# Performance work log

Hardware: AMD Instinct MI355X
Metric: run time of the kernel (lower is better)

Reference implementation:

```python
import jax, jax.numpy as jnp
import numpy as np


def _batched_histc(x, bins):
    # x: [N, ...] -> per-sample histogram over [0, 1], matching torch.histc semantics:
    # bin = floor(v * bins), v == 1.0 goes to last bin, values outside [0,1] ignored.
    N = x.shape[0]
    flat = x.reshape(N, -1)
    idx = jnp.clip((flat * bins).astype(jnp.int32), 0, bins - 1)  # [N, P]
    valid = ((flat >= 0.0) & (flat <= 1.0)).astype(x.dtype)
    gidx = (jnp.arange(N, dtype=jnp.int32)[:, None] * bins + idx).reshape(-1)
    counts = jax.ops.segment_sum(valid.reshape(-1), gidx, num_segments=N * bins)
    return counts.reshape(N, bins)


def _mlp(h, W1, b1, W2, b2, W3, b3, W4, b4):
    h = jax.nn.relu(h @ W1 + b1)
    h = jax.nn.relu(h @ W2 + b2)
    h = jax.nn.relu(h @ W3 + b3)
    return h @ W4 + b4  # [N, 1]


def setup_inputs() -> dict:
    key = jax.random.key(0)
    ks = jax.random.split(key, 5)
    bins = 128
    N, C, H, W = 128, 1, 1024, 1024
    x = jax.random.uniform(ks[0], (N, C, H, W), dtype=jnp.float32)
    def lin(k, fan_in, fan_out):
        s = 1.0 / np.sqrt(fan_in)
        return jax.random.uniform(k, (fan_in, fan_out), jnp.float32, -s, s)
    return {
        "x": x,
        "W1": lin(ks[1], bins, 32), "b1": jnp.zeros((32,), jnp.float32),
        "W2": lin(ks[2], 32, 64),   "b2": jnp.zeros((64,), jnp.float32),
        "W3": lin(ks[3], 64, 128),  "b3": jnp.zeros((128,), jnp.float32),
        "W4": lin(ks[4], 128, 1),   "b4": jnp.zeros((1,), jnp.float32),
        "bins": bins,
    }


def reference(x, W1, b1, W2, b2, W3, b3, W4, b4, bins):
    hst = _batched_histc(x, bins)                       # [N, bins]
    w = _mlp(hst, W1, b1, W2, b2, W3, b3, W4, b4)       # [N, 1]
    w = w[:, :, None, None]                             # [N, 1, 1, 1]
    return x * w
```

## Files before the change

### kernel.cpp

```cpp
#include <hip/hip_runtime.h>

#define N_IMG 128
#define BINS 128
#define HW_ELEMS (1 << 20)
#define PARTS 8
#define NBLOCKS (N_IMG * PARTS)
#define PART_ELEMS (HW_ELEMS / PARTS)
#define PART_V4 (PART_ELEMS / 4)
#define NCOPY 8
#define HPAD 132
#define WSTRIDE 16

typedef float f32x4 __attribute__((ext_vector_type(4)));

__device__ __forceinline__ void ag_store(int* p, int v) {
    __hip_atomic_store(p, v, __ATOMIC_RELAXED, __HIP_MEMORY_SCOPE_AGENT);
}
__device__ __forceinline__ int ag_load(const int* p) {
    return __hip_atomic_load(p, __ATOMIC_RELAXED, __HIP_MEMORY_SCOPE_AGENT);
}
__device__ __forceinline__ int rmw_inc(int* p) {
    return __hip_atomic_fetch_add(p, 1, __ATOMIC_RELAXED, __HIP_MEMORY_SCOPE_AGENT);
}
__device__ __forceinline__ void st_w64(unsigned long long* p, unsigned long long v) {
    __hip_atomic_store(p, v, __ATOMIC_RELAXED, __HIP_MEMORY_SCOPE_AGENT);
}
__device__ __forceinline__ unsigned long long ld_w64(const unsigned long long* p) {
    return __hip_atomic_load(p, __ATOMIC_RELAXED, __HIP_MEMORY_SCOPE_AGENT);
}

__global__ __launch_bounds__(256, 4) void fused_kernel(
    const float* __restrict__ x,
    const float* __restrict__ W1, const float* __restrict__ b1,
    const float* __restrict__ W2, const float* __restrict__ b2,
    const float* __restrict__ W3, const float* __restrict__ b3,
    const float* __restrict__ W4, const float* __restrict__ b4,
    float* __restrict__ out,
    int* __restrict__ parthist,
    int* __restrict__ done,
    unsigned long long* __restrict__ wflag)
{
    __shared__ int   lh[NCOPY * HPAD];
    __shared__ float h0[BINS], a1[32], a2[64], a3[BINS];
    __shared__ int   retsh;
    __shared__ float wbc;

    const int t    = threadIdx.x;
    const int cpy  = t >> 5;
    const int img  = blockIdx.x >> 3;
    const int part = blockIdx.x & (PARTS - 1);

    for (int i = t; i < NCOPY * HPAD; i += 256) lh[i] = 0;
    __syncthreads();

    const f32x4* src = (const f32x4*)(x + (size_t)img * HW_ELEMS
                                        + (size_t)part * PART_ELEMS);

    #pragma unroll 4
    for (int i = t; i < PART_V4; i += 256) {
        f32x4 v = src[i];
        #pragma unroll
        for (int k = 0; k < 4; ++k) {
            float f = v[k];
            if (f >= 0.0f && f <= 1.0f) {
                int b = (int)(f * 128.0f);
                b = b > 127 ? 127 : b;
                atomicAdd(&lh[cpy * HPAD + b], 1);
            }
        }
    }
    __syncthreads();

    if (t < BINS) {
        int s = 0;
        #pragma unroll
        for (int c = 0; c < NCOPY; ++c) s += lh[c * HPAD + t];
        ag_store(&parthist[((size_t)img * PARTS + part) * BINS + t], s);
    }
    __syncthreads();
    if (t == 0) retsh = rmw_inc(&done[img]);
    __syncthreads();

    if (retsh == PARTS - 1) {
        if (t < BINS) {
            int s = 0;
            #pragma unroll
            for (int p = 0; p < PARTS; ++p)
                s += ag_load(&parthist[((size_t)img * PARTS + p) * BINS + t]);
            h0[t] = (float)s;
        }
        __syncthreads();
        if (t < 32) {
            float acc = b1[t];
            #pragma unroll 8
            for (int i = 0; i < 128; ++i) acc += h0[i] * W1[i * 32 + t];
            a1[t] = fmaxf(acc, 0.0f);
        }
        __syncthreads();
        if (t < 64) {
            float acc = b2[t];
            #pragma unroll 8
            for (int i = 0; i < 32; ++i) acc += a1[i] * W2[i * 64 + t];
            a2[t] = fmaxf(acc, 0.0f);
        }
        __syncthreads();
        if (t < 128) {
            float acc = b3[t];
            #pragma unroll 8
            for (int i = 0; i < 64; ++i) acc += a2[i] * W3[i * 128 + t];
            a3[t] = fmaxf(acc, 0.0f);
        }
        __syncthreads();
        if (t < 64) {
            float p = a3[t] * W4[t] + a3[t + 64] * W4[t + 64];
            #pragma unroll
            for (int off = 32; off > 0; off >>= 1)
                p += __shfl_down(p, off, 64);
            if (t == 0) {
                unsigned long long fv =
                    ((unsigned long long)__float_as_uint(p + b4[0]) << 32) | 1ull;
                st_w64(&wflag[(size_t)img * WSTRIDE], fv);
            }
        }
    }

    if (t == 0) {
        unsigned long long fv;
        while (((fv = ld_w64(&wflag[(size_t)img * WSTRIDE])) & 1ull) == 0ull)
            __builtin_amdgcn_s_sleep(16);
        wbc = __uint_as_float((unsigned)(fv >> 32));
    }
    __syncthreads();
    const float w = wbc;

    f32x4* dst = (f32x4*)(out + (size_t)img * HW_ELEMS
                              + (size_t)part * PART_ELEMS);
    #pragma unroll 4
    for (int i = t; i < PART_V4; i += 256) {
        f32x4 v = src[i];
        v *= w;
        __builtin_nontemporal_store(v, &dst[i]);
    }
}

extern "C" void kernel_launch(void* const* d_in, const int* in_sizes, int n_in,
                              void* d_out, int out_size, void* d_ws, size_t ws_size,
                              hipStream_t stream) {
    const float* x  = (const float*)d_in[0];
    const float* W1 = (const float*)d_in[1];
    const float* b1 = (const float*)d_in[2];
    const float* W2 = (const float*)d_in[3];
    const float* b2 = (const float*)d_in[4];
    const float* W3 = (const float*)d_in[5];
    const float* b3 = (const float*)d_in[6];
    const float* W4 = (const float*)d_in[7];
    const float* b4 = (const float*)d_in[8];

    int* done = (int*)d_ws;
    unsigned long long* wflag = (unsigned long long*)(done + N_IMG);
    int* parthist = (int*)(wflag + (size_t)N_IMG * WSTRIDE);

    hipMemsetAsync(d_ws, 0,
                   N_IMG * sizeof(int) + (size_t)N_IMG * WSTRIDE * sizeof(unsigned long long),
                   stream);

    fused_kernel<<<NBLOCKS, 256, 0, stream>>>(x, W1, b1, W2, b2, W3, b3, W4, b4,
                                              (float*)d_out, parthist, done, wflag);
}
```

Baseline: 322.3 us.

## Schedule scaling tiles by weight completion order and use per-quad histogram copies

The scaling pass is no longer tied to the block's own image. Each finished image's weight is pushed into a ring in completion order, and all blocks pull 128 KB tiles from eight atomic counters and scale tiles of whichever images are ready. This is meant to stop blocks spinning while waiting for a specific image's MLP. The shared histogram is also split into 64 copies, one per 4 threads, to cut atomic contention. The cost is more shared memory per block, which may lower occupancy, plus extra global atomics and barriers per tile.

```diff
diff --git a/kernel.cpp b/kernel.cpp
--- a/kernel.cpp
+++ b/kernel.cpp
@@ -7,9 +7,14 @@
 #define NBLOCKS (N_IMG * PARTS)
 #define PART_ELEMS (HW_ELEMS / PARTS)
 #define PART_V4 (PART_ELEMS / 4)
-#define NCOPY 8
+#define NCOPY 64
 #define HPAD 132
-#define WSTRIDE 16
+#define TILES_PER_IMG 32
+#define TILE_ELEMS (HW_ELEMS / TILES_PER_IMG)
+#define TILE_V4 (TILE_ELEMS / 4)
+#define TOTAL_TILES (N_IMG * TILES_PER_IMG)
+#define NGRP 8
+#define TPG (TOTAL_TILES / NGRP)
 
 typedef float f32x4 __attribute__((ext_vector_type(4)));
 
@@ -28,6 +33,13 @@
 __device__ __forceinline__ unsigned long long ld_w64(const unsigned long long* p) {
     return __hip_atomic_load(p, __ATOMIC_RELAXED, __HIP_MEMORY_SCOPE_AGENT);
 }
+
+#define OFF_DONE 0
+#define OFF_TAIL 128
+#define OFF_CTR  160
+#define OFF_RING 416
+#define RING_STRIDE 16
+#define OFF_PART (416 + N_IMG * RING_STRIDE * 2)
 
 __global__ __launch_bounds__(256, 4) void fused_kernel(
     const float* __restrict__ x,
@@ -35,27 +47,31 @@
     const float* __restrict__ W2, const float* __restrict__ b2,
     const float* __restrict__ W3, const float* __restrict__ b3,
     const float* __restrict__ W4, const float* __restrict__ b4,
-    float* __restrict__ out,
-    int* __restrict__ parthist,
-    int* __restrict__ done,
-    unsigned long long* __restrict__ wflag)
+    float* __restrict__ out, int* __restrict__ ws)
 {
     __shared__ int   lh[NCOPY * HPAD];
     __shared__ float h0[BINS], a1[32], a2[64], a3[BINS];
-    __shared__ int   retsh;
-    __shared__ float wbc;
+    __shared__ int   retsh, ksh, imgsh;
+    __shared__ float wsh;
+
+    int* done = ws + OFF_DONE;
+    int* tail = ws + OFF_TAIL;
+    int* ctr  = ws + OFF_CTR;
+    unsigned long long* ring = (unsigned long long*)(ws + OFF_RING);
+    int* parthist = ws + OFF_PART;
 
     const int t    = threadIdx.x;
-    const int cpy  = t >> 5;
-    const int img  = blockIdx.x >> 3;
-    const int part = blockIdx.x & (PARTS - 1);
+    const int g    = blockIdx.x;
+    const int cpy  = t >> 2;
+    const int img  = g >> 3;
+    const int part = g & (PARTS - 1);
 
     for (int i = t; i < NCOPY * HPAD; i += 256) lh[i] = 0;
     __syncthreads();
 
     const f32x4* src = (const f32x4*)(x + (size_t)img * HW_ELEMS
                                         + (size_t)part * PART_ELEMS);
-
+    int* myh = &lh[cpy * HPAD];
     #pragma unroll 4
     for (int i = t; i < PART_V4; i += 256) {
         f32x4 v = src[i];
@@ -65,7 +81,7 @@
             if (f >= 0.0f && f <= 1.0f) {
                 int b = (int)(f * 128.0f);
                 b = b > 127 ? 127 : b;
-                atomicAdd(&lh[cpy * HPAD + b], 1);
+                atomicAdd(&myh[b], 1);
             }
         }
     }
@@ -117,29 +133,53 @@
             for (int off = 32; off > 0; off >>= 1)
                 p += __shfl_down(p, off, 64);
             if (t == 0) {
+                float w = p + b4[0];
+                int pos = rmw_inc(tail);
                 unsigned long long fv =
-                    ((unsigned long long)__float_as_uint(p + b4[0]) << 32) | 1ull;
-                st_w64(&wflag[(size_t)img * WSTRIDE], fv);
-            }
-        }
-    }
-
-    if (t == 0) {
-        unsigned long long fv;
-        while (((fv = ld_w64(&wflag[(size_t)img * WSTRIDE])) & 1ull) == 0ull)
-            __builtin_amdgcn_s_sleep(16);
-        wbc = __uint_as_float((unsigned)(fv >> 32));
-    }
-    __syncthreads();
-    const float w = wbc;
-
-    f32x4* dst = (f32x4*)(out + (size_t)img * HW_ELEMS
-                              + (size_t)part * PART_ELEMS);
-    #pragma unroll 4
-    for (int i = t; i < PART_V4; i += 256) {
-        f32x4 v = src[i];
-        v *= w;
-        __builtin_nontemporal_store(v, &dst[i]);
+                    ((unsigned long long)__float_as_uint(w) << 32)
+                    | ((unsigned)img << 1) | 1ull;
+                st_w64(&ring[(size_t)pos * RING_STRIDE], fv);
+            }
+        }
+        __syncthreads();
+    }
+
+    const int c0 = g & (NGRP - 1);
+    for (int gi = 0; gi < NGRP; ++gi) {
+        const int c = (c0 + gi) & (NGRP - 1);
+        for (;;) {
+            if (t == 0) ksh = rmw_inc(&ctr[c * 32]);
+            __syncthreads();
+            const int k = ksh;
+            __syncthreads();
+            if (k >= TPG) break;
+            const int tile = k * NGRP + c;
+            const int slot = tile >> 5;
+            const int sub  = tile & (TILES_PER_IMG - 1);
+
+            if (t == 0) {
+                unsigned long long fv;
+                while (((fv = ld_w64(&ring[(size_t)slot * RING_STRIDE])) & 1ull) == 0ull)
+                    __builtin_amdgcn_s_sleep(8);
+                imgsh = (int)((fv >> 1) & 0x7f);
+                wsh   = __uint_as_float((unsigned)(fv >> 32));
+            }
+            __syncthreads();
+            const int   tim = imgsh;
+            const float w   = wsh;
+
+            const f32x4* s4 = (const f32x4*)(x + (size_t)tim * HW_ELEMS
+                                               + (size_t)sub * TILE_ELEMS);
+            f32x4* d4 = (f32x4*)(out + (size_t)tim * HW_ELEMS
+                                     + (size_t)sub * TILE_ELEMS);
+            #pragma unroll 8
+            for (int i = t; i < TILE_V4; i += 256) {
+                f32x4 v = s4[i];
+                v *= w;
+                __builtin_nontemporal_store(v, &d4[i]);
+            }
+            __syncthreads();
+        }
     }
 }
 
@@ -156,14 +196,9 @@
     const float* W4 = (const float*)d_in[7];
     const float* b4 = (const float*)d_in[8];
 
-    int* done = (int*)d_ws;
-    unsigned long long* wflag = (unsigned long long*)(done + N_IMG);
-    int* parthist = (int*)(wflag + (size_t)N_IMG * WSTRIDE);
-
-    hipMemsetAsync(d_ws, 0,
-                   N_IMG * sizeof(int) + (size_t)N_IMG * WSTRIDE * sizeof(unsigned long long),
-                   stream);
+    int* ws = (int*)d_ws;
+    hipMemsetAsync(ws, 0, (size_t)OFF_PART * sizeof(int), stream);
 
     fused_kernel<<<NBLOCKS, 256, 0, stream>>>(x, W1, b1, W2, b2, W3, b3, W4, b4,
-                                              (float*)d_out, parthist, done, wflag);
-}
+                                              (float*)d_out, ws);
+}
```

After: 310.4 us. -3.7%, faster.
